# Kernel optimization log

Hardware: AMD Instinct MI355X
Metric: run time of the kernel (lower is better)

The kernel has to match this reference:

```python
import jax, jax.numpy as jnp
import numpy as np

N_NODES = 100000
D_FEAT = 128
N_EDGES = 1600000
N_CLASSES = 32


def setup_inputs() -> dict:
    key = jax.random.key(0)
    k1, k2, k3, k4 = jax.random.split(key, 4)
    x = jax.random.normal(k1, (N_NODES, D_FEAT), dtype=jnp.float32)
    edge_index = jax.random.randint(k2, (2, N_EDGES), 0, N_NODES, dtype=jnp.int64)
    # Linear(input_feat, classes) params (PyTorch default init scale)
    bound = 1.0 / np.sqrt(D_FEAT)
    W = jax.random.uniform(k3, (N_CLASSES, D_FEAT), minval=-bound, maxval=bound, dtype=jnp.float32)
    b = jax.random.uniform(k4, (N_CLASSES,), minval=-bound, maxval=bound, dtype=jnp.float32)
    return {"x": x, "edge_index": edge_index, "W": W, "b": b}


def reference(x, edge_index, W, b):
    # GINConv: out = mlp((1 + eps) * x + sum_{j in N(i)} x_j), eps = 0 (default)
    src, dst = edge_index[0], edge_index[1]
    # gather source features [E, D] and scatter-add into target nodes [N, D]
    agg = jax.ops.segment_sum(x[src], dst, num_segments=N_NODES)
    h = x + agg  # (1 + eps) * x with eps = 0
    # Linear: [N, D] @ [D, C] + [C]
    return h @ W.T + b
```

## Files before the change

### kernel.cpp

```cpp
#include <hip/hip_runtime.h>

#define N_NODES 100000
#define D_FEAT 128
#define N_CLASSES 32
#define BSHIFT 8
#define NB 391
#define EPB 4096
#define CAPB 4608
#define GCAP 1536

typedef __attribute__((ext_vector_type(8))) short short8;
typedef __attribute__((ext_vector_type(4))) float f32x4;

__device__ __forceinline__ unsigned short f2bf(float f) {
  unsigned u = __float_as_uint(f);
  u += 0x7fffu + ((u >> 16) & 1);
  return (unsigned short)(u >> 16);
}

__global__ __launch_bounds__(256) void gin_prep(const float* __restrict__ W,
                                                unsigned short* __restrict__ Wb,
                                                int* __restrict__ gcount) {
  int i = blockIdx.x * 256 + threadIdx.x;
  if (i < D_FEAT * N_CLASSES) Wb[i] = f2bf(W[i]);
  if (i < NB) gcount[i] = 0;
}

__global__ __launch_bounds__(256) void gin_mid(
    const float* __restrict__ x, const unsigned short* __restrict__ Wb,
    float* __restrict__ y,
    const int* __restrict__ src, const int* __restrict__ dst,
    int* __restrict__ gcount, unsigned* __restrict__ bucketed,
    int E, int GBr) {
  __shared__ int cnt[NB];
  __shared__ int cur[NB];
  __shared__ int loff[NB + 1];
  __shared__ int gbase[NB];
  __shared__ int part[256];
  __shared__ unsigned sorted[EPB];
  __shared__ int gaddr[EPB];
  int tid = threadIdx.x;

  if ((int)blockIdx.x >= GBr) {
    int pb = blockIdx.x - GBr;
    int wave = tid >> 6, lane = tid & 63;
    int node_base = pb * 64 + wave * 16;
    if (node_base >= N_NODES) return;
    int m = lane & 15, quad = lane >> 4;

    short8 bfrag[2][4];
#pragma unroll
    for (int cb = 0; cb < 2; ++cb) {
      const unsigned short* wr = Wb + (cb * 16 + m) * D_FEAT + quad * 8;
#pragma unroll
      for (int ks = 0; ks < 4; ++ks)
        bfrag[cb][ks] = *(const short8*)(wr + ks * 32);
    }

    const float* xr = x + (size_t)(node_base + m) * D_FEAT + quad * 8;
    short8 afrag[4];
#pragma unroll
    for (int ks = 0; ks < 4; ++ks) {
      float4 f0 = *(const float4*)(xr + ks * 32);
      float4 f1 = *(const float4*)(xr + ks * 32 + 4);
      float fl[8] = {f0.x, f0.y, f0.z, f0.w, f1.x, f1.y, f1.z, f1.w};
      short8 a;
#pragma unroll
      for (int j = 0; j < 8; ++j) a[j] = (short)f2bf(fl[j]);
      afrag[ks] = a;
    }

    f32x4 acc0 = {0.f, 0.f, 0.f, 0.f};
    f32x4 acc1 = {0.f, 0.f, 0.f, 0.f};
#pragma unroll
    for (int ks = 0; ks < 4; ++ks) {
      acc0 = __builtin_amdgcn_mfma_f32_16x16x32_bf16(afrag[ks], bfrag[0][ks], acc0, 0, 0, 0);
      acc1 = __builtin_amdgcn_mfma_f32_16x16x32_bf16(afrag[ks], bfrag[1][ks], acc1, 0, 0, 0);
    }

#pragma unroll
    for (int r = 0; r < 4; ++r) {
      int node = node_base + quad * 4 + r;
      y[(size_t)node * N_CLASSES + m] = acc0[r];
      y[(size_t)node * N_CLASSES + 16 + m] = acc1[r];
    }
    return;
  }

  int blk = blockIdx.x;
  for (int i = tid; i < NB; i += 256) {
    cnt[i] = 0;
    cur[i] = 0;
  }
  __syncthreads();
  int base = blk * EPB;
  bool full = (base + EPB <= E);
  if (full) {
#pragma unroll 4
    for (int k = 0; k < EPB / 256; ++k)
      atomicAdd(&cnt[dst[base + k * 256 + tid] >> BSHIFT], 1);
  } else {
    for (int k = 0; k < EPB / 256; ++k) {
      int e = base + k * 256 + tid;
      if (e < E) atomicAdd(&cnt[dst[e] >> BSHIFT], 1);
    }
  }
  __syncthreads();
  for (int i = tid; i < NB; i += 256) {
    int c = cnt[i];
    gbase[i] = c ? atomicAdd(&gcount[i], c) : 0;
  }
  int i0 = tid * 2;
  int v0 = (i0 < NB) ? cnt[i0] : 0;
  int v1 = (i0 + 1 < NB) ? cnt[i0 + 1] : 0;
  int s0 = v0 + v1;
  part[tid] = s0;
  __syncthreads();
  for (int o = 1; o < 256; o <<= 1) {
    int t = (tid >= o) ? part[tid - o] : 0;
    __syncthreads();
    part[tid] += t;
    __syncthreads();
  }
  int run = part[tid] - s0;
  if (i0 < NB) loff[i0] = run;
  if (i0 + 1 < NB) loff[i0 + 1] = run + v0;
  if (tid == 255) loff[NB] = part[255];
  __syncthreads();
  if (full) {
    for (int k = 0; k < EPB / 256; k += 4) {
      int e0 = base + (k + 0) * 256 + tid;
      int e1 = base + (k + 1) * 256 + tid;
      int e2 = base + (k + 2) * 256 + tid;
      int e3 = base + (k + 3) * 256 + tid;
      int d0 = dst[e0], d1 = dst[e1], d2 = dst[e2], d3 = dst[e3];
      unsigned s0v = src[e0], s1v = src[e1], s2v = src[e2], s3v = src[e3];
      int b0 = d0 >> BSHIFT, b1 = d1 >> BSHIFT, b2 = d2 >> BSHIFT, b3 = d3 >> BSHIFT;
      int r0 = atomicAdd(&cur[b0], 1);
      int r1 = atomicAdd(&cur[b1], 1);
      int r2 = atomicAdd(&cur[b2], 1);
      int r3 = atomicAdd(&cur[b3], 1);
      int p0 = loff[b0] + r0, p1 = loff[b1] + r1, p2 = loff[b2] + r2, p3 = loff[b3] + r3;
      int g0 = gbase[b0] + r0, g1 = gbase[b1] + r1, g2 = gbase[b2] + r2, g3 = gbase[b3] + r3;
      sorted[p0] = s0v | ((unsigned)(d0 & 255) << 17);
      gaddr[p0] = (g0 < CAPB) ? (b0 * CAPB + g0) : -1;
      sorted[p1] = s1v | ((unsigned)(d1 & 255) << 17);
      gaddr[p1] = (g1 < CAPB) ? (b1 * CAPB + g1) : -1;
      sorted[p2] = s2v | ((unsigned)(d2 & 255) << 17);
      gaddr[p2] = (g2 < CAPB) ? (b2 * CAPB + g2) : -1;
      sorted[p3] = s3v | ((unsigned)(d3 & 255) << 17);
      gaddr[p3] = (g3 < CAPB) ? (b3 * CAPB + g3) : -1;
    }
  } else {
    for (int k = 0; k < EPB / 256; ++k) {
      int e = base + k * 256 + tid;
      if (e < E) {
        int d = dst[e];
        int bb = d >> BSHIFT;
        int r = atomicAdd(&cur[bb], 1);
        int p = loff[bb] + r;
        int gg = gbase[bb] + r;
        sorted[p] = (unsigned)src[e] | ((unsigned)(d & 255) << 17);
        gaddr[p] = (gg < CAPB) ? (bb * CAPB + gg) : -1;
      }
    }
  }
  __syncthreads();
  int ltot = loff[NB];
#pragma unroll 4
  for (int i = tid; i < ltot; i += 256) {
    int ga = gaddr[i];
    if (ga >= 0) bucketed[ga] = sorted[i];
  }
}

__global__ __launch_bounds__(512) void gin_gather_q(
    const int* __restrict__ gcount, const unsigned* __restrict__ bucketed,
    const float* __restrict__ y, const float* __restrict__ bias,
    float* __restrict__ out) {
  __shared__ unsigned sorted[GCAP];
  __shared__ int cnt[64];
  __shared__ int off[65];
  __shared__ int cur[64];
  int tid = threadIdx.x;
  int bk = blockIdx.x >> 2;
  int qq = blockIdx.x & 3;
  int len = gcount[bk];
  if (len > CAPB) len = CAPB;
  const unsigned* bb = bucketed + (size_t)bk * CAPB;
  if (tid < 64) cnt[tid] = 0;
  __syncthreads();
  for (int i = tid; i < len; i += 512) {
    unsigned p = bb[i];
    int n8 = (int)((p >> 17) & 255u);
    if ((n8 >> 6) == qq) atomicAdd(&cnt[n8 & 63], 1);
  }
  __syncthreads();
  if (tid == 0) off[0] = 0;
  if (tid < 64) off[tid + 1] = cnt[tid];
  __syncthreads();
  for (int o = 1; o < 64; o <<= 1) {
    int v = (tid < 64 && tid >= o) ? off[tid + 1 - o] : 0;
    __syncthreads();
    if (tid < 64) off[tid + 1] += v;
    __syncthreads();
  }
  if (tid < 64) cur[tid] = off[tid];
  __syncthreads();
  for (int i = tid; i < len; i += 512) {
    unsigned p = bb[i];
    int n8 = (int)((p >> 17) & 255u);
    if ((n8 >> 6) == qq) {
      int pos = atomicAdd(&cur[n8 & 63], 1);
      if (pos < GCAP) sorted[pos] = p;
    }
  }
  __syncthreads();
  int g = tid >> 5, lane = tid & 31, q = lane & 7, slot = lane >> 3;
  const float4* y4 = (const float4*)y;
  float4 bq = ((const float4*)bias)[q];
#pragma unroll
  for (int u = 0; u < 4; ++u) {
    int dl = g * 4 + u;
    int es = off[dl], ee = off[dl + 1];
    if (ee > GCAP) ee = GCAP;
    if (es > ee) es = ee;
    float4 acc = make_float4(0.f, 0.f, 0.f, 0.f);
    int it = es + slot;
    for (; it + 12 < ee; it += 16) {
      unsigned p0 = sorted[it], p1 = sorted[it + 4], p2 = sorted[it + 8], p3 = sorted[it + 12];
      float4 w0 = y4[(size_t)(p0 & 0x1FFFF) * 8 + q];
      float4 w1 = y4[(size_t)(p1 & 0x1FFFF) * 8 + q];
      float4 w2 = y4[(size_t)(p2 & 0x1FFFF) * 8 + q];
      float4 w3 = y4[(size_t)(p3 & 0x1FFFF) * 8 + q];
      acc.x += w0.x + w1.x + w2.x + w3.x;
      acc.y += w0.y + w1.y + w2.y + w3.y;
      acc.z += w0.z + w1.z + w2.z + w3.z;
      acc.w += w0.w + w1.w + w2.w + w3.w;
    }
    for (; it < ee; it += 4) {
      unsigned p = sorted[it];
      float4 w = y4[(size_t)(p & 0x1FFFF) * 8 + q];
      acc.x += w.x; acc.y += w.y; acc.z += w.z; acc.w += w.w;
    }
#pragma unroll
    for (int m = 8; m <= 16; m <<= 1) {
      acc.x += __shfl_xor(acc.x, m, 64);
      acc.y += __shfl_xor(acc.y, m, 64);
      acc.z += __shfl_xor(acc.z, m, 64);
      acc.w += __shfl_xor(acc.w, m, 64);
    }
    int node = (bk << 8) + (qq << 6) + dl;
    if (slot == 0 && node < N_NODES) {
      float4 yv = y4[(size_t)node * 8 + q];
      float4 r;
      r.x = acc.x + yv.x + bq.x;
      r.y = acc.y + yv.y + bq.y;
      r.z = acc.z + yv.z + bq.z;
      r.w = acc.w + yv.w + bq.w;
      ((float4*)out)[(size_t)node * 8 + q] = r;
    }
  }
}

__global__ __launch_bounds__(256) void gin_bias_init(
    const float* __restrict__ y, const float* __restrict__ b,
    float* __restrict__ out) {
  int gid = blockIdx.x * 256 + threadIdx.x;
  if (gid < N_NODES * N_CLASSES) out[gid] = y[gid] + b[gid & 31];
}
__global__ __launch_bounds__(256) void gin_scatter_fb(
    const int* __restrict__ src, const int* __restrict__ dst,
    const float* __restrict__ y, float* __restrict__ out, int n_edges) {
  long long gid = (long long)blockIdx.x * 256 + threadIdx.x;
  int e = (int)(gid >> 5);
  int c = (int)(gid & 31);
  if (e >= n_edges) return;
  atomicAdd(&out[(size_t)dst[e] * N_CLASSES + c],
            y[(size_t)src[e] * N_CLASSES + c]);
}

extern "C" void kernel_launch(void* const* d_in, const int* in_sizes, int n_in,
                              void* d_out, int out_size, void* d_ws, size_t ws_size,
                              hipStream_t stream) {
  const float* x = (const float*)d_in[0];
  const int* edge_index = (const int*)d_in[1];
  const float* W = (const float*)d_in[2];
  const float* b = (const float*)d_in[3];
  float* out = (float*)d_out;

  int E = in_sizes[1] / 2;
  const int* src = edge_index;
  const int* dst = edge_index + E;

  int GBr = (E + EPB - 1) / EPB;
  int pblocks = (N_NODES + 63) / 64;

  char* ws = (char*)d_ws;
  size_t sz_y = (size_t)N_NODES * N_CLASSES * 4;
  size_t sz_wb = (D_FEAT * N_CLASSES * 2 + 15) & ~15ull;
  size_t sz_bucketed = (((size_t)NB * CAPB * 4) + 15) & ~15ull;
  size_t sz_gcnt = ((size_t)NB * 4 + 15) & ~15ull;

  float* y = (float*)ws;
  unsigned short* Wb = (unsigned short*)(ws + sz_y);
  unsigned* bucketed = (unsigned*)(ws + sz_y + sz_wb);
  int* gcount = (int*)(ws + sz_y + sz_wb + sz_bucketed);
  size_t need = sz_y + sz_wb + sz_bucketed + sz_gcnt;

  if (ws_size < need) {
    gin_prep<<<16, 256, 0, stream>>>(W, Wb, (int*)ws);
    gin_mid<<<pblocks, 256, 0, stream>>>(x, Wb, y, src, dst, (int*)ws, (unsigned*)ws, E, 0);
    gin_bias_init<<<(N_NODES * N_CLASSES + 255) / 256, 256, 0, stream>>>(y, b, out);
    long long t2 = (long long)E * N_CLASSES;
    gin_scatter_fb<<<(int)((t2 + 255) / 256), 256, 0, stream>>>(src, dst, y, out, E);
    return;
  }

  gin_prep<<<16, 256, 0, stream>>>(W, Wb, gcount);
  gin_mid<<<GBr + pblocks, 256, 0, stream>>>(x, Wb, y, src, dst, gcount, bucketed, E, GBr);
  gin_gather_q<<<NB * 4, 512, 0, stream>>>(gcount, bucketed, y, b, out);
}
```

Baseline: 154.3 us.

## Replace gather-side counting sort with LDS atomic accumulation; keep edges in registers

The bucketing kernel now loads each block's src/dst into registers once and reuses them for both the count and scatter passes. It drops the per-edge global-address array and recovers each bucket by binary search over the local offsets. The gather kernel no longer counting-sorts edges per node. Each 32-lane group reads an edge's projected row and atomically adds it into a 64x32 shared accumulator, removing two passes, a scan and the GCAP cap, at the cost of LDS float atomics and reading the whole bucket in four quarter-blocks.

```diff
diff --git a/kernel.cpp b/kernel.cpp
--- a/kernel.cpp
+++ b/kernel.cpp
@@ -7,7 +7,6 @@
 #define NB 391
 #define EPB 4096
 #define CAPB 4608
-#define GCAP 1536
 
 typedef __attribute__((ext_vector_type(8))) short short8;
 typedef __attribute__((ext_vector_type(4))) float f32x4;
@@ -38,7 +37,6 @@
   __shared__ int gbase[NB];
   __shared__ int part[256];
   __shared__ unsigned sorted[EPB];
-  __shared__ int gaddr[EPB];
   int tid = threadIdx.x;
 
   if ((int)blockIdx.x >= GBr) {
@@ -95,17 +93,27 @@
   __syncthreads();
   int base = blk * EPB;
   bool full = (base + EPB <= E);
+
+  int dv[16];
+  unsigned sv[16];
   if (full) {
-#pragma unroll 4
-    for (int k = 0; k < EPB / 256; ++k)
-      atomicAdd(&cnt[dst[base + k * 256 + tid] >> BSHIFT], 1);
+#pragma unroll
+    for (int k = 0; k < 16; ++k) dv[k] = dst[base + k * 256 + tid];
+#pragma unroll
+    for (int k = 0; k < 16; ++k) sv[k] = (unsigned)src[base + k * 256 + tid];
   } else {
-    for (int k = 0; k < EPB / 256; ++k) {
+#pragma unroll
+    for (int k = 0; k < 16; ++k) {
       int e = base + k * 256 + tid;
-      if (e < E) atomicAdd(&cnt[dst[e] >> BSHIFT], 1);
-    }
-  }
-  __syncthreads();
+      dv[k] = (e < E) ? dst[e] : -1;
+      sv[k] = (e < E) ? (unsigned)src[e] : 0u;
+    }
+  }
+#pragma unroll
+  for (int k = 0; k < 16; ++k)
+    if (dv[k] >= 0) atomicAdd(&cnt[dv[k] >> BSHIFT], 1);
+  __syncthreads();
+
   for (int i = tid; i < NB; i += 256) {
     int c = cnt[i];
     gbase[i] = c ? atomicAdd(&gcount[i], c) : 0;
@@ -127,139 +135,70 @@
   if (i0 + 1 < NB) loff[i0 + 1] = run + v0;
   if (tid == 255) loff[NB] = part[255];
   __syncthreads();
-  if (full) {
-    for (int k = 0; k < EPB / 256; k += 4) {
-      int e0 = base + (k + 0) * 256 + tid;
-      int e1 = base + (k + 1) * 256 + tid;
-      int e2 = base + (k + 2) * 256 + tid;
-      int e3 = base + (k + 3) * 256 + tid;
-      int d0 = dst[e0], d1 = dst[e1], d2 = dst[e2], d3 = dst[e3];
-      unsigned s0v = src[e0], s1v = src[e1], s2v = src[e2], s3v = src[e3];
-      int b0 = d0 >> BSHIFT, b1 = d1 >> BSHIFT, b2 = d2 >> BSHIFT, b3 = d3 >> BSHIFT;
-      int r0 = atomicAdd(&cur[b0], 1);
-      int r1 = atomicAdd(&cur[b1], 1);
-      int r2 = atomicAdd(&cur[b2], 1);
-      int r3 = atomicAdd(&cur[b3], 1);
-      int p0 = loff[b0] + r0, p1 = loff[b1] + r1, p2 = loff[b2] + r2, p3 = loff[b3] + r3;
-      int g0 = gbase[b0] + r0, g1 = gbase[b1] + r1, g2 = gbase[b2] + r2, g3 = gbase[b3] + r3;
-      sorted[p0] = s0v | ((unsigned)(d0 & 255) << 17);
-      gaddr[p0] = (g0 < CAPB) ? (b0 * CAPB + g0) : -1;
-      sorted[p1] = s1v | ((unsigned)(d1 & 255) << 17);
-      gaddr[p1] = (g1 < CAPB) ? (b1 * CAPB + g1) : -1;
-      sorted[p2] = s2v | ((unsigned)(d2 & 255) << 17);
-      gaddr[p2] = (g2 < CAPB) ? (b2 * CAPB + g2) : -1;
-      sorted[p3] = s3v | ((unsigned)(d3 & 255) << 17);
-      gaddr[p3] = (g3 < CAPB) ? (b3 * CAPB + g3) : -1;
-    }
-  } else {
-    for (int k = 0; k < EPB / 256; ++k) {
-      int e = base + k * 256 + tid;
-      if (e < E) {
-        int d = dst[e];
-        int bb = d >> BSHIFT;
-        int r = atomicAdd(&cur[bb], 1);
-        int p = loff[bb] + r;
-        int gg = gbase[bb] + r;
-        sorted[p] = (unsigned)src[e] | ((unsigned)(d & 255) << 17);
-        gaddr[p] = (gg < CAPB) ? (bb * CAPB + gg) : -1;
-      }
-    }
-  }
-  __syncthreads();
+
+#pragma unroll
+  for (int k = 0; k < 16; ++k) {
+    if (dv[k] >= 0) {
+      int b = dv[k] >> BSHIFT;
+      int r = atomicAdd(&cur[b], 1);
+      sorted[loff[b] + r] = sv[k] | ((unsigned)(dv[k] & 255) << 17);
+    }
+  }
+  __syncthreads();
+
   int ltot = loff[NB];
-#pragma unroll 4
   for (int i = tid; i < ltot; i += 256) {
-    int ga = gaddr[i];
-    if (ga >= 0) bucketed[ga] = sorted[i];
-  }
-}
-
-__global__ __launch_bounds__(512) void gin_gather_q(
+    int lo = 0, hi = NB;
+    while (hi - lo > 1) {
+      int md = (lo + hi) >> 1;
+      if (loff[md] <= i) lo = md; else hi = md;
+    }
+    int ga = gbase[lo] + (i - loff[lo]);
+    if (ga < CAPB) bucketed[(size_t)lo * CAPB + ga] = sorted[i];
+  }
+}
+
+__global__ __launch_bounds__(512) void gin_gather_acc(
     const int* __restrict__ gcount, const unsigned* __restrict__ bucketed,
     const float* __restrict__ y, const float* __restrict__ bias,
     float* __restrict__ out) {
-  __shared__ unsigned sorted[GCAP];
-  __shared__ int cnt[64];
-  __shared__ int off[65];
-  __shared__ int cur[64];
+  __shared__ float acc[64 * 32];
   int tid = threadIdx.x;
   int bk = blockIdx.x >> 2;
   int qq = blockIdx.x & 3;
   int len = gcount[bk];
   if (len > CAPB) len = CAPB;
   const unsigned* bb = bucketed + (size_t)bk * CAPB;
-  if (tid < 64) cnt[tid] = 0;
-  __syncthreads();
-  for (int i = tid; i < len; i += 512) {
-    unsigned p = bb[i];
-    int n8 = (int)((p >> 17) & 255u);
-    if ((n8 >> 6) == qq) atomicAdd(&cnt[n8 & 63], 1);
-  }
-  __syncthreads();
-  if (tid == 0) off[0] = 0;
-  if (tid < 64) off[tid + 1] = cnt[tid];
-  __syncthreads();
-  for (int o = 1; o < 64; o <<= 1) {
-    int v = (tid < 64 && tid >= o) ? off[tid + 1 - o] : 0;
-    __syncthreads();
-    if (tid < 64) off[tid + 1] += v;
-    __syncthreads();
-  }
-  if (tid < 64) cur[tid] = off[tid];
-  __syncthreads();
-  for (int i = tid; i < len; i += 512) {
+  for (int i = tid; i < 64 * 32; i += 512) acc[i] = 0.f;
+  __syncthreads();
+  int grp = tid >> 5, lane = tid & 31;
+#pragma unroll 2
+  for (int i = grp; i < len; i += 16) {
     unsigned p = bb[i];
     int n8 = (int)((p >> 17) & 255u);
     if ((n8 >> 6) == qq) {
-      int pos = atomicAdd(&cur[n8 & 63], 1);
-      if (pos < GCAP) sorted[pos] = p;
-    }
-  }
-  __syncthreads();
-  int g = tid >> 5, lane = tid & 31, q = lane & 7, slot = lane >> 3;
+      float v = y[(size_t)(p & 0x1FFFF) * 32 + lane];
+      atomicAdd(&acc[(n8 & 63) * 32 + lane], v);
+    }
+  }
+  __syncthreads();
+  int base_node = (bk << 8) + (qq << 6);
   const float4* y4 = (const float4*)y;
-  float4 bq = ((const float4*)bias)[q];
-#pragma unroll
-  for (int u = 0; u < 4; ++u) {
-    int dl = g * 4 + u;
-    int es = off[dl], ee = off[dl + 1];
-    if (ee > GCAP) ee = GCAP;
-    if (es > ee) es = ee;
-    float4 acc = make_float4(0.f, 0.f, 0.f, 0.f);
-    int it = es + slot;
-    for (; it + 12 < ee; it += 16) {
-      unsigned p0 = sorted[it], p1 = sorted[it + 4], p2 = sorted[it + 8], p3 = sorted[it + 12];
-      float4 w0 = y4[(size_t)(p0 & 0x1FFFF) * 8 + q];
-      float4 w1 = y4[(size_t)(p1 & 0x1FFFF) * 8 + q];
-      float4 w2 = y4[(size_t)(p2 & 0x1FFFF) * 8 + q];
-      float4 w3 = y4[(size_t)(p3 & 0x1FFFF) * 8 + q];
-      acc.x += w0.x + w1.x + w2.x + w3.x;
-      acc.y += w0.y + w1.y + w2.y + w3.y;
-      acc.z += w0.z + w1.z + w2.z + w3.z;
-      acc.w += w0.w + w1.w + w2.w + w3.w;
-    }
-    for (; it < ee; it += 4) {
-      unsigned p = sorted[it];
-      float4 w = y4[(size_t)(p & 0x1FFFF) * 8 + q];
-      acc.x += w.x; acc.y += w.y; acc.z += w.z; acc.w += w.w;
-    }
-#pragma unroll
-    for (int m = 8; m <= 16; m <<= 1) {
-      acc.x += __shfl_xor(acc.x, m, 64);
-      acc.y += __shfl_xor(acc.y, m, 64);
-      acc.z += __shfl_xor(acc.z, m, 64);
-      acc.w += __shfl_xor(acc.w, m, 64);
-    }
-    int node = (bk << 8) + (qq << 6) + dl;
-    if (slot == 0 && node < N_NODES) {
-      float4 yv = y4[(size_t)node * 8 + q];
-      float4 r;
-      r.x = acc.x + yv.x + bq.x;
-      r.y = acc.y + yv.y + bq.y;
-      r.z = acc.z + yv.z + bq.z;
-      r.w = acc.w + yv.w + bq.w;
-      ((float4*)out)[(size_t)node * 8 + q] = r;
-    }
+  const float4* b4 = (const float4*)bias;
+  const float4* a4 = (const float4*)acc;
+  int i = tid;
+  int node = base_node + (i >> 3);
+  int q = i & 7;
+  if (node < N_NODES) {
+    float4 a = a4[i];
+    float4 yv = y4[(size_t)node * 8 + q];
+    float4 bq = b4[q];
+    float4 r;
+    r.x = a.x + yv.x + bq.x;
+    r.y = a.y + yv.y + bq.y;
+    r.z = a.z + yv.z + bq.z;
+    r.w = a.w + yv.w + bq.w;
+    ((float4*)out)[(size_t)node * 8 + q] = r;
   }
 }
 
@@ -319,5 +258,5 @@
 
   gin_prep<<<16, 256, 0, stream>>>(W, Wb, gcount);
   gin_mid<<<GBr + pblocks, 256, 0, stream>>>(x, Wb, y, src, dst, gcount, bucketed, E, GBr);
-  gin_gather_q<<<NB * 4, 512, 0, stream>>>(gcount, bucketed, y, b, out);
-}
+  gin_gather_acc<<<NB * 4, 512, 0, stream>>>(gcount, bucketed, y, b, out);
+}
```

After: 435.1 us. 182% more time.
